# Kernel optimization log

Measured on AMD Instinct MI355X. Metric: run time of the kernel, lower is better.

Reference implementation:

```python
import jax, jax.numpy as jnp
import numpy as np

B, S, E, H = 4, 2048, 1024, 16
DH = E // H
EXP = 1024  # FeedForwardPart default expansion_dim
EPS = 1e-5


def layer_norm(x, gamma, beta):
    mu = jnp.mean(x, axis=-1, keepdims=True)
    var = jnp.var(x, axis=-1, keepdims=True)
    return (x - mu) * jax.lax.rsqrt(var + EPS) * gamma + beta


def setup_inputs() -> dict:
    key = jax.random.key(0)
    ks = jax.random.split(key, 8)
    s = 0.02
    return {
        "x": jax.random.normal(ks[0], (B, S, E), jnp.float32),
        "mask": jnp.ones((B, 1, 1, S), jnp.int32),
        "wq": jax.random.normal(ks[1], (E, E), jnp.float32) * s,
        "wk": jax.random.normal(ks[2], (E, E), jnp.float32) * s,
        "wv": jax.random.normal(ks[3], (E, E), jnp.float32) * s,
        "wo": jax.random.normal(ks[4], (E, E), jnp.float32) * s,
        "bo": jnp.zeros((E,), jnp.float32),
        "w1": jax.random.normal(ks[5], (E, EXP), jnp.float32) * s,
        "b1": jnp.zeros((EXP,), jnp.float32),
        "w2": jax.random.normal(ks[6], (EXP, E), jnp.float32) * s,
        "b2": jnp.zeros((E,), jnp.float32),
        "gamma": jnp.ones((E,), jnp.float32),
        "beta": jnp.zeros((E,), jnp.float32),
    }


def reference(x, mask, wq, wk, wv, wo, bo, w1, b1, w2, b2, gamma, beta):
    # Multi-head self-attention
    q = (x @ wq).reshape(B, S, H, DH)
    k = (x @ wk).reshape(B, S, H, DH)
    v = (x @ wv).reshape(B, S, H, DH)
    scores = jnp.einsum("bqhd,bkhd->bhqk", q, k) / jnp.sqrt(jnp.float32(DH))
    scores = jnp.where(mask == 0, jnp.float32(-1e10), scores)
    attn = jax.nn.softmax(scores, axis=-1)
    ctx = jnp.einsum("bhqk,bkhd->bqhd", attn, v).reshape(B, S, E)
    attn_out = ctx @ wo + bo
    # Residual + shared LayerNorm
    h = layer_norm(attn_out + x, gamma, beta)
    # FFN (expansion 1024 per source default)
    ff = jax.nn.relu(h @ w1 + b1) @ w2 + b2
    return layer_norm(ff + h, gamma, beta)
```

## Files before the change

kernel.cpp:

```cpp
#include <hip/hip_runtime.h>
#include <hip/hip_bf16.h>

typedef short s16x8 __attribute__((ext_vector_type(8)));
typedef float f32x4 __attribute__((ext_vector_type(4)));
typedef float f32x16 __attribute__((ext_vector_type(16)));
typedef unsigned short u16;

#define B_ 4
#define S_ 2048
#define E_ 1024
#define H_ 16
#define DH_ 64

__device__ __forceinline__ u16 f2b(float f) {
  union { float f; unsigned u; } x; x.f = f;
  unsigned r = (x.u + 0x7fffu + ((x.u >> 16) & 1u)) >> 16;
  return (u16)r;
}

__device__ __forceinline__ float b2f(u16 v) {
  union { unsigned u; float f; } x; x.u = ((unsigned)v) << 16; return x.f;
}

__device__ __forceinline__ unsigned pk2(float lo, float hi) {
  __hip_bfloat162 h = __float22bfloat162_rn(float2{lo, hi});
  union { __hip_bfloat162 h; unsigned u; } c; c.h = h; return c.u;
}

__device__ __forceinline__ float fexp2(float x) { return __builtin_amdgcn_exp2f(x); }

__device__ __forceinline__ float max3f(float a, float b, float c) {
  return fmaxf(fmaxf(a, b), c);
}

__device__ __forceinline__ void pl32swap(unsigned& x, unsigned& y) {
  asm("v_permlane32_swap_b32 %0, %1" : "+v"(x), "+v"(y));
}

__device__ __forceinline__ float pmax32(float v) {
  union { float f; unsigned u; } a, b;
  a.f = v; b.f = v;
  pl32swap(a.u, b.u);
  return fmaxf(a.f, b.f);
}

__device__ __forceinline__ void async16(const void* g, void* l) {
  __builtin_amdgcn_global_load_lds((const __attribute__((address_space(1))) void*)g,
                                   (__attribute__((address_space(3))) void*)l,
                                   16, 0, 0);
}

__global__ __launch_bounds__(256) void k_cast(const float* __restrict__ in,
                                              u16* __restrict__ out, int n4) {
  int i = blockIdx.x * 256 + threadIdx.x;
  if (i >= n4) return;
  float4 v = ((const float4*)in)[i];
  ushort4 o;
  o.x = f2b(v.x); o.y = f2b(v.y); o.z = f2b(v.z); o.w = f2b(v.w);
  ((ushort4*)out)[i] = o;
}

__global__ __launch_bounds__(256) void k_castT6(
    const float* __restrict__ w0, const float* __restrict__ w1,
    const float* __restrict__ w2, const float* __restrict__ w3,
    const float* __restrict__ w4, const float* __restrict__ w5,
    u16* __restrict__ wtBase) {
  __shared__ float tile[32][33];
  const int z = blockIdx.z;
  const float* in = z == 0 ? w0 : z == 1 ? w1 : z == 2 ? w2 : z == 3 ? w3 : z == 4 ? w4 : w5;
  u16* out = wtBase + (size_t)z * (1024 * 1024);
  int k0 = blockIdx.x * 32, n0 = blockIdx.y * 32;
  int tx = threadIdx.x, ty = threadIdx.y;
#pragma unroll
  for (int i = 0; i < 32; i += 8)
    tile[ty + i][tx] = in[(long)(k0 + ty + i) * 1024 + n0 + tx];
  __syncthreads();
#pragma unroll
  for (int i = 0; i < 32; i += 8)
    out[(long)(n0 + ty + i) * 1024 + k0 + tx] = f2b(tile[tx][ty + i]);
}

__global__ __launch_bounds__(256, 2) void k_gemm(
    const u16* __restrict__ A, const u16* __restrict__ Bt,
    int N, int K,
    const float* __restrict__ bias, int relu, int mode,
    float* __restrict__ outF, u16* __restrict__ outB,
    u16* __restrict__ oq, u16* __restrict__ ok, u16* __restrict__ ov) {
  __shared__ __align__(16) u16 Al[128 * 32];
  __shared__ __align__(16) u16 Bl[128 * 32];
  const int t = threadIdx.x;
  const int lane = t & 63, w = t >> 6;
  const int g = lane >> 4, li = lane & 15;
  const int wr = w >> 1, wc = w & 1;
  const int bm = blockIdx.x * 128, bn = blockIdx.y * 128;

  f32x4 acc[4][4] = {};

  const long ar0 = bm + (t >> 2), ar1 = bm + ((256 + t) >> 2);
  const long br0 = bn + (t >> 2), br1 = bn + ((256 + t) >> 2);
  const int c0 = (t & 3) * 8, c1 = ((256 + t) & 3) * 8;
  u16* aD0 = &Al[(w * 64) * 8];
  u16* aD1 = &Al[(256 + w * 64) * 8];
  u16* bD0 = &Bl[(w * 64) * 8];
  u16* bD1 = &Bl[(256 + w * 64) * 8];

  for (int kt = 0; kt < K; kt += 32) {
    async16(&A[ar0 * K + kt + c0], aD0);
    async16(&A[ar1 * K + kt + c1], aD1);
    async16(&Bt[br0 * K + kt + c0], bD0);
    async16(&Bt[br1 * K + kt + c1], bD1);
    __syncthreads();
    s16x8 af[4], bf[4];
#pragma unroll
    for (int mi = 0; mi < 4; ++mi)
      af[mi] = *(const s16x8*)&Al[(wr * 64 + mi * 16 + li) * 32 + g * 8];
#pragma unroll
    for (int nf = 0; nf < 4; ++nf)
      bf[nf] = *(const s16x8*)&Bl[(wc * 64 + nf * 16 + li) * 32 + g * 8];
#pragma unroll
    for (int mi = 0; mi < 4; ++mi)
#pragma unroll
      for (int nf = 0; nf < 4; ++nf)
        acc[mi][nf] = __builtin_amdgcn_mfma_f32_16x16x32_bf16(af[mi], bf[nf], acc[mi][nf], 0, 0, 0);
    __syncthreads();
  }

#pragma unroll
  for (int mi = 0; mi < 4; ++mi)
#pragma unroll
    for (int nf = 0; nf < 4; ++nf) {
      int col = bn + wc * 64 + nf * 16 + li;
      if (mode == 1) {
        int which = col >> 10, cc = col & 1023;
        int hh = cc >> 6, dd = cc & 63;
        u16* dst = which == 0 ? oq : (which == 1 ? ok : ov);
        float scl = which == 0 ? 0.18033688011112042f : 1.f;
#pragma unroll
        for (int r = 0; r < 4; ++r) {
          long row = bm + wr * 64 + mi * 16 + g * 4 + r;
          int b2 = (int)(row >> 11), ss = (int)(row & 2047);
          dst[(((long)b2 * H_ + hh) * S_ + ss) * DH_ + dd] = f2b(acc[mi][nf][r] * scl);
        }
      } else {
        float bv = bias ? bias[col] : 0.f;
#pragma unroll
        for (int r = 0; r < 4; ++r) {
          long row = bm + wr * 64 + mi * 16 + g * 4 + r;
          float v = acc[mi][nf][r] + bv;
          if (relu) v = fmaxf(v, 0.f);
          if (outF) outF[row * N + col] = v;
          if (outB) outB[row * N + col] = f2b(v);
        }
      }
    }
}

__global__ __launch_bounds__(512) void k_attn(
    const u16* __restrict__ Q, const u16* __restrict__ Kg, const u16* __restrict__ Vg,
    const int* __restrict__ mask, u16* __restrict__ ctx) {
  __shared__ __align__(16) u16 Kl[3][64 * 64];
  __shared__ __align__(16) u16 Vt[3][64 * 72];
  __shared__ __align__(16) float MBs[S_];
  __shared__ int MFlag[S_ / 64];
  __shared__ __align__(16) float BC[8 * 32];
  const int t = threadIdx.x;
  const int lane = t & 63, wid = t >> 6;
  const int q = lane & 31, hi = lane >> 5;
  const int bh = blockIdx.x;
  const int b = bh >> 4, h = bh & 15;
  const long bhoff = (long)bh * S_ * DH_;
  const int q0 = blockIdx.y * 256 + wid * 32;
  const int skey = t >> 3, sdj = t & 7;
  const int NT = S_ / 64;

  {
    int4 m4 = ((const int4*)(mask + (long)b * S_))[t];
    float4 f;
    f.x = m4.x ? 0.f : -1e10f; f.y = m4.y ? 0.f : -1e10f;
    f.z = m4.z ? 0.f : -1e10f; f.w = m4.w ? 0.f : -1e10f;
    ((float4*)MBs)[t] = f;
    bool ok = m4.x && m4.y && m4.z && m4.w;
    unsigned long long vote = __ballot(ok);
    if ((lane & 15) == 0)
      MFlag[t >> 4] = (((vote >> ((lane >> 4) * 16)) & 0xFFFFull) == 0xFFFFull);
  }

  s16x8 qf[4];
  {
    const u16* Qp = Q + bhoff + (long)(q0 + q) * DH_;
#pragma unroll
    for (int c = 0; c < 4; ++c) qf[c] = *(const s16x8*)(Qp + c * 16 + hi * 8);
  }

  s16x8 onesv;
#pragma unroll
  for (int j = 0; j < 8; ++j) onesv[j] = (short)0x3F80;

  s16x8 kreg, vreg;
#define LOADKV(TI) { \
    kreg = *(const s16x8*)(Kg + bhoff + (long)((TI) * 64 + skey) * DH_ + sdj * 8); \
    vreg = *(const s16x8*)(Vg + bhoff + (long)((TI) * 64 + lane) * DH_ + wid * 8); }
#define WRITEKV(BUF) { \
    *(s16x8*)((char*)&Kl[BUF][0] + skey * 128 + ((sdj * 16) ^ ((skey & 7) << 4))) = kreg; \
    _Pragma("unroll") \
    for (int j = 0; j < 8; ++j) Vt[BUF][(wid * 8 + j) * 72 + lane] = (u16)vreg[j]; }

  const int swz = (q & 7) << 4;
#define QKSTEP(S0, S1, BUF) { \
    const char* Kc = (const char*)&Kl[BUF][0]; \
    _Pragma("unroll") \
    for (int c = 0; c < 4; ++c) { \
      s16x8 kf0 = *(const s16x8*)(Kc + q * 128 + ((c * 32 + hi * 16) ^ swz)); \
      s16x8 kf1 = *(const s16x8*)(Kc + (32 + q) * 128 + ((c * 32 + hi * 16) ^ swz)); \
      S0 = __builtin_amdgcn_mfma_f32_32x32x16_bf16(kf0, qf[c], S0, 0, 0, 0); \
      S1 = __builtin_amdgcn_mfma_f32_32x32x16_bf16(kf1, qf[c], S1, 0, 0, 0); \
    } }

#define SOFTPV(S0, S1, TI) { \
    const int kt = (TI) * 64; \
    const u16* Vc = &Vt[(TI) % 3][0]; \
    if (MFlag[TI] == 0) {   \
      _Pragma("unroll") \
      for (int g4 = 0; g4 < 4; ++g4) { \
        f32x4 mb0 = *(const f32x4*)&MBs[kt + g4 * 8 + hi * 4]; \
        f32x4 mb1 = *(const f32x4*)&MBs[kt + 32 + g4 * 8 + hi * 4]; \
        _Pragma("unroll") \
        for (int e = 0; e < 4; ++e) { \
          S0[g4 * 4 + e] += mb0[e]; S1[g4 * 4 + e] += mb1[e]; \
        } \
      } \
    } \
    float u0 = max3f(S0[0], S0[1], S0[2]); \
    float u1 = max3f(S0[3], S0[4], S0[5]); \
    float u2 = max3f(S0[6], S0[7], S0[8]); \
    float u3 = max3f(S0[9], S0[10], S0[11]); \
    float u4 = max3f(S0[12], S0[13], S0[14]); \
    float u5 = max3f(S0[15], S1[0], S1[1]); \
    float u6 = max3f(S1[2], S1[3], S1[4]); \
    float u7 = max3f(S1[5], S1[6], S1[7]); \
    float u8 = max3f(S1[8], S1[9], S1[10]); \
    float u9 = max3f(S1[11], S1[12], S1[13]); \
    float ua = fmaxf(S1[14], S1[15]); \
    float w0 = max3f(u0, u1, u2), w1 = max3f(u3, u4, u5); \
    float w2 = max3f(u6, u7, u8), w3 = max3f(u9, ua, w0); \
    float tmax = pmax32(max3f(w1, w2, w3)); \
    if (!__all(tmax <= m_run + 11.5f)) { \
      float mnew = fmaxf(m_run, tmax); \
      float corr = fexp2(m_run - mnew); \
      m_run = mnew; \
      if (lane < 32) BC[wid * 32 + q] = corr; \
      asm volatile("s_waitcnt lgkmcnt(0)" ::: "memory"); \
      _Pragma("unroll") \
      for (int g4 = 0; g4 < 4; ++g4) { \
        f32x4 cv = *(const f32x4*)&BC[wid * 32 + g4 * 8 + hi * 4]; \
        _Pragma("unroll") \
        for (int e = 0; e < 4; ++e) { \
          o0[g4 * 4 + e] *= cv[e]; o1[g4 * 4 + e] *= cv[e]; ol[g4 * 4 + e] *= cv[e]; \
        } \
      } \
    } \
    float p[32]; \
    _Pragma("unroll") \
    for (int j = 0; j < 16; ++j) { \
      p[j] = fexp2(S0[j] - m_run); \
      p[16 + j] = fexp2(S1[j] - m_run); \
    } \
    _Pragma("unroll") \
    for (int c = 0; c < 4; ++c) { \
      unsigned X1 = pk2(p[c * 8 + 0], p[c * 8 + 1]); \
      unsigned X2 = pk2(p[c * 8 + 2], p[c * 8 + 3]); \
      unsigned Y1 = pk2(p[c * 8 + 4], p[c * 8 + 5]); \
      unsigned Y2 = pk2(p[c * 8 + 6], p[c * 8 + 7]); \
      pl32swap(X1, Y1); pl32swap(X2, Y2); \
      union { unsigned u[4]; s16x8 v; } pu; \
      pu.u[0] = X1; pu.u[1] = X2; pu.u[2] = Y1; pu.u[3] = Y2; \
      s16x8 vb0 = *(const s16x8*)(Vc + (long)q * 72 + c * 16 + hi * 8); \
      s16x8 vb1 = *(const s16x8*)(Vc + (long)(32 + q) * 72 + c * 16 + hi * 8); \
      o0 = __builtin_amdgcn_mfma_f32_32x32x16_bf16(pu.v, vb0, o0, 0, 0, 0); \
      o1 = __builtin_amdgcn_mfma_f32_32x32x16_bf16(pu.v, vb1, o1, 0, 0, 0); \
      ol = __builtin_amdgcn_mfma_f32_32x32x16_bf16(pu.v, onesv, ol, 0, 0, 0); \
    } }

#define ITER(I, SC0, SC1, SN0, SN1) { \
    const int ip1 = (I) + 1; \
    if (ip1 < NT) WRITEKV(ip1 % 3); \
    __syncthreads(); \
    if (ip1 < NT) { \
      SN0 = zz; SN1 = zz; \
      QKSTEP(SN0, SN1, ip1 % 3); \
      if (ip1 + 1 < NT) LOADKV(ip1 + 1); \
    } \
    SOFTPV(SC0, SC1, I); }

  f32x16 zz = {};
  f32x16 o0 = zz, o1 = zz, ol = zz;
  float m_run = -1e30f;

  LOADKV(0);
  WRITEKV(0);
  __syncthreads();
  f32x16 sA0 = zz, sA1 = zz, sB0 = zz, sB1 = zz;
  QKSTEP(sA0, sA1, 0);
  LOADKV(1);

  for (int i = 0; i < NT; i += 2) {
    ITER(i, sA0, sA1, sB0, sB1);
    ITER(i + 1, sB0, sB1, sA0, sA1);
  }

#pragma unroll
  for (int g4 = 0; g4 < 4; ++g4)
#pragma unroll
    for (int e = 0; e < 4; ++e) {
      int qr = e + g4 * 8 + hi * 4;
      float inv = 1.f / fmaxf(ol[g4 * 4 + e], 1e-30f);
      long ro = ((long)(b * S_ + q0 + qr) * H_ + h) * DH_ + q;
      ctx[ro] = f2b(o0[g4 * 4 + e] * inv);
      ctx[ro + 32] = f2b(o1[g4 * 4 + e] * inv);
    }
#undef LOADKV
#undef WRITEKV
#undef QKSTEP
#undef SOFTPV
#undef ITER
}

__global__ __launch_bounds__(256) void k_lnb(const u16* __restrict__ a, const u16* __restrict__ res,
                                             const float* __restrict__ gamma, const float* __restrict__ beta,
                                             float* __restrict__ outF, u16* __restrict__ outB) {
  const int row = blockIdx.x, t = threadIdx.x;
  const long base = (long)row * E_;
  ushort4 av = ((const ushort4*)(a + base))[t];
  float4 s = make_float4(b2f(av.x), b2f(av.y), b2f(av.z), b2f(av.w));
  if (res) {
    ushort4 rv = ((const ushort4*)(res + base))[t];
    s.x += b2f(rv.x); s.y += b2f(rv.y); s.z += b2f(rv.z); s.w += b2f(rv.w);
  }
  float ps = s.x + s.y + s.z + s.w;
  float pq = s.x * s.x + s.y * s.y + s.z * s.z + s.w * s.w;
#pragma unroll
  for (int xm = 32; xm >= 1; xm >>= 1) { ps += __shfl_xor(ps, xm); pq += __shfl_xor(pq, xm); }
  __shared__ float red[8];
  int w = t >> 6, lane = t & 63;
  if (lane == 0) { red[w] = ps; red[4 + w] = pq; }
  __syncthreads();
  ps = red[0] + red[1] + red[2] + red[3];
  pq = red[4] + red[5] + red[6] + red[7];
  float mu = ps * (1.f / E_);
  float rs = rsqrtf(pq * (1.f / E_) - mu * mu + 1e-5f);
  float4 gv = ((const float4*)gamma)[t];
  float4 be = ((const float4*)beta)[t];
  float4 o = make_float4((s.x - mu) * rs * gv.x + be.x, (s.y - mu) * rs * gv.y + be.y,
                         (s.z - mu) * rs * gv.z + be.z, (s.w - mu) * rs * gv.w + be.w);
  if (outF) ((float4*)(outF + base))[t] = o;
  if (outB) {
    ushort4 ob; ob.x = f2b(o.x); ob.y = f2b(o.y); ob.z = f2b(o.z); ob.w = f2b(o.w);
    ((ushort4*)(outB + base))[t] = ob;
  }
}

extern "C" void kernel_launch(void* const* d_in, const int* in_sizes, int n_in,
                              void* d_out, int out_size, void* d_ws, size_t ws_size,
                              hipStream_t stream) {
  const float* x  = (const float*)d_in[0];
  const int* mask = (const int*)d_in[1];
  const float* wq = (const float*)d_in[2];
  const float* wk = (const float*)d_in[3];
  const float* wv = (const float*)d_in[4];
  const float* wo = (const float*)d_in[5];
  const float* bo = (const float*)d_in[6];
  const float* w1 = (const float*)d_in[7];
  const float* b1 = (const float*)d_in[8];
  const float* w2 = (const float*)d_in[9];
  const float* b2 = (const float*)d_in[10];
  const float* gamma = (const float*)d_in[11];
  const float* beta  = (const float*)d_in[12];
  float* out = (float*)d_out;

  char* ws = (char*)d_ws;
  const size_t MB = 1024ull * 1024ull;
  u16* xb  = (u16*)(ws + 0);
  u16* wqt = (u16*)(ws + 16 * MB);
  u16* wot = (u16*)(ws + 22 * MB);
  u16* w1t = (u16*)(ws + 24 * MB);
  u16* w2t = (u16*)(ws + 26 * MB);
  u16* qb  = (u16*)(ws + 28 * MB);
  u16* kb  = (u16*)(ws + 44 * MB);
  u16* vb  = (u16*)(ws + 60 * MB);
  u16* ctx = (u16*)(ws + 76 * MB);
  u16* aob = (u16*)(ws + 92 * MB);
  u16* hb  = (u16*)(ws + 108 * MB);
  u16* ff1 = qb;
  u16* ff2b = kb;

  const int n4 = B_ * S_ * E_ / 4;
  k_cast<<<n4 / 256, 256, 0, stream>>>(x, xb, n4);
  k_castT6<<<dim3(32, 32, 6), dim3(32, 8), 0, stream>>>(wq, wk, wv, wo, w1, w2, wqt);

  k_gemm<<<dim3(64, 24), 256, 0, stream>>>(xb, wqt, 3072, 1024, nullptr, 0, 1,
                                           nullptr, nullptr, qb, kb, vb);

  k_attn<<<dim3(B_ * H_, S_ / 256), 512, 0, stream>>>(qb, kb, vb, mask, ctx);

  dim3 gg(64, 8);
  k_gemm<<<gg, 256, 0, stream>>>(ctx, wot, 1024, 1024, bo, 0, 0, nullptr, aob,
                                 nullptr, nullptr, nullptr);
  k_lnb<<<B_ * S_, 256, 0, stream>>>(aob, xb, gamma, beta, nullptr, hb);
  k_gemm<<<gg, 256, 0, stream>>>(hb, w1t, 1024, 1024, b1, 1, 0, nullptr, ff1,
                                 nullptr, nullptr, nullptr);
  k_gemm<<<gg, 256, 0, stream>>>(ff1, w2t, 1024, 1024, b2, 0, 0, nullptr, ff2b,
                                 nullptr, nullptr, nullptr);
  k_lnb<<<B_ * S_, 256, 0, stream>>>(ff2b, hb, gamma, beta, out, nullptr);
}
```

Measured before the change: 301.9 us.

## Store V transposed from QKV GEMM and async-stage K/V tiles in attention

The QKV projection GEMM now writes V in a head-major transposed layout [b,h,d,s], staging it through shared memory so global stores are 16-byte vectorized. This lets the attention kernel load both K and V tiles with direct async global-to-LDS copies into XOR-swizzled buffers two tiles ahead. That replaces the register round trip and the scalar transposing LDS writes for V. It costs extra LDS and barriers in the GEMM epilogue, and adds a full vmcnt(0) wait at every attention iteration.

```diff
diff --git a/kernel.cpp b/kernel.cpp
--- a/kernel.cpp
+++ b/kernel.cpp
@@ -88,6 +88,7 @@
     u16* __restrict__ oq, u16* __restrict__ ok, u16* __restrict__ ov) {
   __shared__ __align__(16) u16 Al[128 * 32];
   __shared__ __align__(16) u16 Bl[128 * 32];
+  __shared__ __align__(16) u16 VT[64][136];
   const int t = threadIdx.x;
   const int lane = t & 63, w = t >> 6;
   const int g = lane >> 4, li = lane & 15;
@@ -125,6 +126,32 @@
     __syncthreads();
   }
 
+  if (mode == 1 && bn >= 2048) {
+    const int hv0 = (bn - 2048) >> 6;
+    const int b2 = (int)(bm >> 11), ss0 = (int)(bm & 2047);
+#pragma unroll 1
+    for (int half = 0; half < 2; ++half) {
+      __syncthreads();
+      if (wc == half) {
+#pragma unroll
+        for (int nf = 0; nf < 4; ++nf)
+#pragma unroll
+          for (int mi = 0; mi < 4; ++mi)
+#pragma unroll
+            for (int r = 0; r < 4; ++r)
+              VT[nf * 16 + li][wr * 64 + mi * 16 + g * 4 + r] = f2b(acc[mi][nf][r]);
+      }
+      __syncthreads();
+      const int colL = t >> 2, seg = t & 3;
+      u16* dst = ov + (((long)b2 * H_ + hv0 + half) * DH_ + colL) * (long)S_ + ss0 + seg * 32;
+      const u16* srcp = &VT[colL][seg * 32];
+#pragma unroll
+      for (int jj = 0; jj < 4; ++jj)
+        ((s16x8*)dst)[jj] = ((const s16x8*)srcp)[jj];
+    }
+    return;
+  }
+
 #pragma unroll
   for (int mi = 0; mi < 4; ++mi)
 #pragma unroll
@@ -133,7 +160,7 @@
       if (mode == 1) {
         int which = col >> 10, cc = col & 1023;
         int hh = cc >> 6, dd = cc & 63;
-        u16* dst = which == 0 ? oq : (which == 1 ? ok : ov);
+        u16* dst = which == 0 ? oq : ok;
         float scl = which == 0 ? 0.18033688011112042f : 1.f;
 #pragma unroll
         for (int r = 0; r < 4; ++r) {
@@ -159,7 +186,7 @@
     const u16* __restrict__ Q, const u16* __restrict__ Kg, const u16* __restrict__ Vg,
     const int* __restrict__ mask, u16* __restrict__ ctx) {
   __shared__ __align__(16) u16 Kl[3][64 * 64];
-  __shared__ __align__(16) u16 Vt[3][64 * 72];
+  __shared__ __align__(16) u16 Vl[3][64 * 64];
   __shared__ __align__(16) float MBs[S_];
   __shared__ int MFlag[S_ / 64];
   __shared__ __align__(16) float BC[8 * 32];
@@ -170,7 +197,6 @@
   const int b = bh >> 4, h = bh & 15;
   const long bhoff = (long)bh * S_ * DH_;
   const int q0 = blockIdx.y * 256 + wid * 32;
-  const int skey = t >> 3, sdj = t & 7;
   const int NT = S_ / 64;
 
   {
@@ -196,14 +222,14 @@
 #pragma unroll
   for (int j = 0; j < 8; ++j) onesv[j] = (short)0x3F80;
 
-  s16x8 kreg, vreg;
-#define LOADKV(TI) { \
-    kreg = *(const s16x8*)(Kg + bhoff + (long)((TI) * 64 + skey) * DH_ + sdj * 8); \
-    vreg = *(const s16x8*)(Vg + bhoff + (long)((TI) * 64 + lane) * DH_ + wid * 8); }
-#define WRITEKV(BUF) { \
-    *(s16x8*)((char*)&Kl[BUF][0] + skey * 128 + ((sdj * 16) ^ ((skey & 7) << 4))) = kreg; \
-    _Pragma("unroll") \
-    for (int j = 0; j < 8; ++j) Vt[BUF][(wid * 8 + j) * 72 + lane] = (u16)vreg[j]; }
+  const int skey = t >> 3, sc8 = t & 7;
+  const u16* Ksrc = Kg + bhoff + (long)skey * DH_ + ((sc8 ^ (skey & 7)) * 8);
+  const u16* Vsrc = Vg + bhoff + (long)skey * S_ + ((sc8 ^ (skey & 7)) * 8);
+
+#define STAGE(TI) { \
+    const int bsel = (TI) % 3; \
+    async16(Ksrc + (long)(TI) * (64 * DH_), (char*)&Kl[bsel][0] + wid * 1024); \
+    async16(Vsrc + (TI) * 64,               (char*)&Vl[bsel][0] + wid * 1024); }
 
   const int swz = (q & 7) << 4;
 #define QKSTEP(S0, S1, BUF) { \
@@ -218,7 +244,7 @@
 
 #define SOFTPV(S0, S1, TI) { \
     const int kt = (TI) * 64; \
-    const u16* Vc = &Vt[(TI) % 3][0]; \
+    const char* Vc = (const char*)&Vl[(TI) % 3][0]; \
     if (MFlag[TI] == 0) {   \
       _Pragma("unroll") \
       for (int g4 = 0; g4 < 4; ++g4) { \
@@ -274,21 +300,21 @@
       pl32swap(X1, Y1); pl32swap(X2, Y2); \
       union { unsigned u[4]; s16x8 v; } pu; \
       pu.u[0] = X1; pu.u[1] = X2; pu.u[2] = Y1; pu.u[3] = Y2; \
-      s16x8 vb0 = *(const s16x8*)(Vc + (long)q * 72 + c * 16 + hi * 8); \
-      s16x8 vb1 = *(const s16x8*)(Vc + (long)(32 + q) * 72 + c * 16 + hi * 8); \
+      s16x8 vb0 = *(const s16x8*)(Vc + q * 128 + ((c * 32 + hi * 16) ^ swz)); \
+      s16x8 vb1 = *(const s16x8*)(Vc + (32 + q) * 128 + ((c * 32 + hi * 16) ^ swz)); \
       o0 = __builtin_amdgcn_mfma_f32_32x32x16_bf16(pu.v, vb0, o0, 0, 0, 0); \
       o1 = __builtin_amdgcn_mfma_f32_32x32x16_bf16(pu.v, vb1, o1, 0, 0, 0); \
       ol = __builtin_amdgcn_mfma_f32_32x32x16_bf16(pu.v, onesv, ol, 0, 0, 0); \
     } }
 
 #define ITER(I, SC0, SC1, SN0, SN1) { \
-    const int ip1 = (I) + 1; \
-    if (ip1 < NT) WRITEKV(ip1 % 3); \
+    const int ip1 = (I) + 1, ip2 = (I) + 2; \
+    asm volatile("s_waitcnt vmcnt(0)" ::: "memory"); \
     __syncthreads(); \
+    if (ip2 < NT) STAGE(ip2); \
     if (ip1 < NT) { \
       SN0 = zz; SN1 = zz; \
       QKSTEP(SN0, SN1, ip1 % 3); \
-      if (ip1 + 1 < NT) LOADKV(ip1 + 1); \
     } \
     SOFTPV(SC0, SC1, I); }
 
@@ -296,12 +322,12 @@
   f32x16 o0 = zz, o1 = zz, ol = zz;
   float m_run = -1e30f;
 
-  LOADKV(0);
-  WRITEKV(0);
+  STAGE(0);
+  STAGE(1);
+  asm volatile("s_waitcnt vmcnt(2)" ::: "memory");
   __syncthreads();
   f32x16 sA0 = zz, sA1 = zz, sB0 = zz, sB1 = zz;
   QKSTEP(sA0, sA1, 0);
-  LOADKV(1);
 
   for (int i = 0; i < NT; i += 2) {
     ITER(i, sA0, sA1, sB0, sB1);
@@ -318,8 +344,7 @@
       ctx[ro] = f2b(o0[g4 * 4 + e] * inv);
       ctx[ro + 32] = f2b(o1[g4 * 4 + e] * inv);
     }
-#undef LOADKV
-#undef WRITEKV
+#undef STAGE
 #undef QKSTEP
 #undef SOFTPV
 #undef ITER
```

Result: slower. 312.3 us (+3.4%).
